# Kernel optimization log

Measured on AMD Instinct MI355X. Metric: run time of the kernel, lower is better.

The kernel has to match this reference:

```python
import jax, jax.numpy as jnp
import numpy as np

B, T, D = 64, 512, 1024   # batch, seq, input_dim
R, O = 1024, 1024          # recurrent_dim, output_dim


def setup_inputs() -> dict:
    key = jax.random.key(0)
    ks = jax.random.split(key, 8)
    s_in = 1.0 / np.sqrt(D)
    s_rec = 1.0 / np.sqrt(R)
    return {
        "x": jax.random.normal(ks[0], (B, T, D), dtype=jnp.float32),
        "Wxh": jax.random.uniform(ks[1], (R, D), jnp.float32, -s_in, s_in),
        "bh": jax.random.uniform(ks[2], (R,), jnp.float32, -s_in, s_in),
        "Whh": jax.random.uniform(ks[3], (R, R), jnp.float32, -s_rec, s_rec),
        "Wxz": jax.random.uniform(ks[4], (R, D), jnp.float32, -s_in, s_in),
        "bz": jax.random.uniform(ks[5], (R,), jnp.float32, -s_in, s_in),
        "Whz": jax.random.uniform(ks[6], (R, R), jnp.float32, -s_rec, s_rec),
        "Wy": jax.random.uniform(ks[7], (O, R), jnp.float32, -s_rec, s_rec),
        "by": jnp.zeros((O,), dtype=jnp.float32),
    }


def reference(x, Wxh, bh, Whh, Wxz, bz, Whz, Wy, by):
    # Original per-step math (note the quirk: h2z output is added to x_t
    # BEFORE x2z):
    #   z  = sigmoid(Wxz @ (x_t + Whz @ h) + bz)
    #   hb = relu(Wxh @ x_t + bh + Whh @ h)
    #   h  = z * h + (1 - z) * hb
    # Precompute all input-side GEMMs in one batched contraction (linearity);
    # fold Wxz@Whz into a single recurrent matrix.
    xh = jnp.einsum('btd,rd->btr', x, Wxh) + bh          # [B,T,R]
    xz = jnp.einsum('btd,rd->btr', x, Wxz) + bz          # [B,T,R]
    Mz = Wxz @ Whz                                        # [R,R]

    def step(h, inp):
        xh_t, xz_t = inp                                  # each [B,R]
        z = jax.nn.sigmoid(xz_t + h @ Mz.T)
        hb = jax.nn.relu(xh_t + h @ Whh.T)
        h = z * h + (1.0 - z) * hb
        return h, None

    h0 = jnp.zeros((x.shape[0], Whh.shape[0]), dtype=x.dtype)
    # scan over time: move T to leading axis
    h_final, _ = jax.lax.scan(
        step, h0, (jnp.swapaxes(xh, 0, 1), jnp.swapaxes(xz, 0, 1)))
    return h_final @ Wy.T + by                            # [B,O]
```

## Files before the change

### kernel.cpp

```cpp
#include <hip/hip_runtime.h>

#define BB 64
#define TT 512
#define DD 1024
#define RR 1024

#define SCAN_BLOCKS 32
#define HS_STRIDE 1032
#define SCAN_LDS_BYTES (64 * HS_STRIDE * 2)

typedef __bf16 bf16x8 __attribute__((ext_vector_type(8)));
typedef float f32x4 __attribute__((ext_vector_type(4)));
typedef unsigned short us4 __attribute__((ext_vector_type(4)));
typedef unsigned int u32x4 __attribute__((ext_vector_type(4)));
typedef unsigned long long u64;

__device__ inline unsigned short f2bf(float f) {
  unsigned int u = __float_as_uint(f);
  u = (u + 0x7fffu + ((u >> 16) & 1u)) >> 16;
  return (unsigned short)u;
}
__device__ inline float bf2f(unsigned short b) {
  return __uint_as_float(((unsigned int)b) << 16);
}

__device__ inline u32x4 ld16_sc(const void* p) {
  u32x4 r;
  asm volatile("global_load_dwordx4 %0, %1, off sc0 sc1"
               : "=v"(r) : "v"(p) : "memory");
  return r;
}

__global__ void k_f2b4(const float* __restrict__ in, unsigned short* __restrict__ out, int n4) {
  int i = blockIdx.x * blockDim.x + threadIdx.x;
  if (i < n4) {
    const float4 v = ((const float4*)in)[i];
    us4 o;
    o.x = f2bf(v.x); o.y = f2bf(v.y); o.z = f2bf(v.z); o.w = f2bf(v.w);
    ((us4*)out)[i] = o;
  }
}

__global__ __launch_bounds__(256) void k_transpose_bf16(
    const float* __restrict__ in, unsigned short* __restrict__ out) {
  __shared__ float tile[32][33];
  const int bx = blockIdx.x * 32, by0 = blockIdx.y * 32;
  const int tx = threadIdx.x, ty = threadIdx.y;
#pragma unroll
  for (int r = 0; r < 32; r += 8)
    tile[ty + r][tx] = in[(size_t)(by0 + ty + r) * 1024 + bx + tx];
  __syncthreads();
#pragma unroll
  for (int r = 0; r < 32; r += 8)
    out[(size_t)(bx + ty + r) * 1024 + by0 + tx] = f2bf(tile[tx][ty + r]);
}

__device__ inline void gload_lds16(const unsigned short* g, unsigned short* l) {
  __builtin_amdgcn_global_load_lds(
      (const __attribute__((address_space(1))) unsigned int*)g,
      (__attribute__((address_space(3))) unsigned int*)l, 16, 0, 0);
}

template <int EPI>
__global__ __launch_bounds__(256) void gemm_bt(
    const unsigned short* __restrict__ A,
    const unsigned short* __restrict__ Bm,
    const float* __restrict__ bias_h,
    const float* __restrict__ bias_z,
    unsigned short* __restrict__ outb, int K) {
  __shared__ __attribute__((aligned(16))) unsigned short As[128 * 32];
  __shared__ __attribute__((aligned(16))) unsigned short Bs[128 * 32];
  const int tid = threadIdx.x;
  const int m0 = blockIdx.y * 128, n0 = blockIdx.x * 128;
  const int lane = tid & 63, wid = tid >> 6;
  const int l16 = lane & 15, quad = lane >> 4;
  const int wm = (wid & 1) * 64, wn = (wid >> 1) * 64;

  f32x4 acc[4][4] = {};

  const int c0 = tid, c1 = 256 + tid;
  const int rowA0 = c0 >> 2, colA0 = (c0 & 3) << 3;
  const int rowA1 = c1 >> 2, colA1 = (c1 & 3) << 3;

  for (int kk = 0; kk < K; kk += 32) {
    __syncthreads();
    gload_lds16(A + (size_t)(m0 + rowA0) * K + kk + colA0, As + c0 * 8);
    gload_lds16(A + (size_t)(m0 + rowA1) * K + kk + colA1, As + c1 * 8);
    gload_lds16(Bm + (size_t)(n0 + rowA0) * K + kk + colA0, Bs + c0 * 8);
    gload_lds16(Bm + (size_t)(n0 + rowA1) * K + kk + colA1, Bs + c1 * 8);
    __syncthreads();
    bf16x8 af[4], bfr[4];
#pragma unroll
    for (int i = 0; i < 4; ++i) {
      af[i] = *(const bf16x8*)&As[(wm + i * 16 + l16) * 32 + quad * 8];
      bfr[i] = *(const bf16x8*)&Bs[(wn + i * 16 + l16) * 32 + quad * 8];
    }
#pragma unroll
    for (int i = 0; i < 4; ++i)
#pragma unroll
      for (int j = 0; j < 4; ++j)
        acc[i][j] = __builtin_amdgcn_mfma_f32_16x16x32_bf16(af[i], bfr[j], acc[i][j], 0, 0, 0);
  }

#pragma unroll
  for (int i = 0; i < 4; ++i) {
#pragma unroll
    for (int j = 0; j < 4; ++j) {
#pragma unroll
      for (int r = 0; r < 4; ++r) {
        const int m = m0 + wm + i * 16 + quad * 4 + r;
        const int n = n0 + wn + j * 16 + l16;
        float v = acc[i][j][r];
        if (EPI == 0) {
          v += (n < 1024) ? bias_h[n] : bias_z[n - 1024];
          const int b = m >> 9;
          const int t = m & 511;
          outb[((size_t)(t * 64 + b) << 11) + n] = f2bf(v);
        } else {
          outb[(size_t)m * 1024 + n] = f2bf(v);
        }
      }
    }
  }
}

__global__ __launch_bounds__(1024) void scan_out_k(
    const unsigned short* __restrict__ xhz,
    const unsigned short* __restrict__ Wrec,
    const unsigned short* __restrict__ Wyb,
    const float* __restrict__ by,
    unsigned short* __restrict__ hb0, unsigned short* __restrict__ hb1,
    unsigned int* __restrict__ flags,
    float* __restrict__ out) {
  extern __shared__ char smem[];
  unsigned short* hs = (unsigned short*)smem;
  float* red = (float*)smem;

  const int tid = threadIdx.x, g = blockIdx.x;
  const int lane = tid & 63, wid = tid >> 6;
  const int l16 = lane & 15, quad = lane >> 4;
  const int ks = wid >> 2, nsub = wid & 3;
  const int kw = ks * 256;
  const int i0 = g * 32;

  const int bcol = (nsub < 2) ? (i0 + nsub * 16 + l16)
                              : (1024 + i0 + (nsub - 2) * 16 + l16);
  const unsigned short* Bb = Wrec + (size_t)bcol * 1024 + kw + quad * 8;
  bf16x8 bfr[8];
#pragma unroll
  for (int s = 0; s < 8; ++s) bfr[s] = *(const bf16x8*)(Bb + s * 32);

  const int sr = tid >> 4;
  const int su = tid & 15;
  const unsigned short* gsrc_base0 = hb0 + sr * 1024 + su * 8;
  const unsigned short* gsrc_base1 = hb1 + sr * 1024 + su * 8;
  unsigned short* ldst = hs + sr * HS_STRIDE + su * 8;

  const int eb = tid >> 4, ej = (tid & 15) * 2;
  float hold0 = 0.0f, hold1 = 0.0f;

  const unsigned short* hbc = hb0;
  unsigned short* hbn = hb1;
  const unsigned short* gsrc = gsrc_base0;

  for (int tt = 0; tt < TT; ++tt) {
    u32x4 tmp[8];
#pragma unroll
    for (int c = 0; c < 8; ++c)
      tmp[c] = ld16_sc((const char*)gsrc + c * 256);
    const size_t xrow = ((size_t)(tt * 64 + eb)) << 11;
    const unsigned int xh2 = *(const unsigned int*)(xhz + xrow + i0 + ej);
    const unsigned int xz2 = *(const unsigned int*)(xhz + xrow + 1024 + i0 + ej);
    asm volatile("s_waitcnt vmcnt(0)" ::: "memory");
#pragma unroll
    for (int c = 0; c < 8; ++c)
      *(u32x4*)(ldst + c * 128) = tmp[c];
    __syncthreads();

    f32x4 acc[4] = {};
#pragma unroll
    for (int s = 0; s < 8; ++s) {
#pragma unroll
      for (int mt = 0; mt < 4; ++mt) {
        const bf16x8 afr = *(const bf16x8*)(hs + (mt * 16 + l16) * HS_STRIDE + kw + s * 32 + quad * 8);
        acc[mt] = __builtin_amdgcn_mfma_f32_16x16x32_bf16(afr, bfr[s], acc[mt], 0, 0, 0);
      }
    }
    __syncthreads();

#pragma unroll
    for (int mt = 0; mt < 4; ++mt)
#pragma unroll
      for (int r = 0; r < 4; ++r)
        red[(size_t)(ks * 64 + mt * 16 + quad * 4 + r) * 68 + nsub * 16 + l16] = acc[mt][r];
    __syncthreads();

    float ph0 = 0.f, ph1 = 0.f, pz0 = 0.f, pz1 = 0.f;
#pragma unroll
    for (int w = 0; w < 4; ++w) {
      const float* rb = red + (size_t)(w * 64 + eb) * 68;
      ph0 += rb[ej]; ph1 += rb[ej + 1];
      pz0 += rb[32 + ej]; pz1 += rb[32 + ej + 1];
    }
    {
      const float xh0 = bf2f((unsigned short)(xh2 & 0xffff));
      const float xh1 = bf2f((unsigned short)(xh2 >> 16));
      const float xz0 = bf2f((unsigned short)(xz2 & 0xffff));
      const float xz1 = bf2f((unsigned short)(xz2 >> 16));
      const float z0 = 1.0f / (1.0f + __expf(-(xz0 + pz0)));
      const float z1 = 1.0f / (1.0f + __expf(-(xz1 + pz1)));
      const float hb_0 = fmaxf(xh0 + ph0, 0.0f);
      const float hb_1 = fmaxf(xh1 + ph1, 0.0f);
      hold0 = z0 * hold0 + (1.0f - z0) * hb_0;
      hold1 = z1 * hold1 + (1.0f - z1) * hb_1;
      const unsigned int pk = (unsigned int)f2bf(hold0) | ((unsigned int)f2bf(hold1) << 16);
      __hip_atomic_store((unsigned int*)(hbn + eb * 1024 + i0 + ej), pk,
                         __ATOMIC_RELAXED, __HIP_MEMORY_SCOPE_AGENT);
    }

    __syncthreads();
    if (tid == 0)
      __hip_atomic_store(&flags[g], (unsigned int)(tt + 1),
                         __ATOMIC_RELAXED, __HIP_MEMORY_SCOPE_AGENT);
    if (tid < 64) {
      const unsigned int tgt = (unsigned int)(tt + 1);
      unsigned int v;
      do {
        v = __hip_atomic_load(&flags[tid & 31], __ATOMIC_RELAXED, __HIP_MEMORY_SCOPE_AGENT);
      } while (__any(v < tgt));
    }
    __syncthreads();

    const unsigned short* tc = hbc; hbc = hbn; hbn = (unsigned short*)tc;
    gsrc = (tt & 1) ? gsrc_base0 : gsrc_base1;
  }

  {
    u32x4 tmp[8];
#pragma unroll
    for (int c = 0; c < 8; ++c)
      tmp[c] = ld16_sc((const char*)(hbc + sr * 1024 + su * 8) + c * 256);
    asm volatile("s_waitcnt vmcnt(0)" ::: "memory");
#pragma unroll
    for (int c = 0; c < 8; ++c)
      *(u32x4*)(ldst + c * 128) = tmp[c];
  }
  __syncthreads();

  if (nsub < 2) {
    const int ocol = i0 + nsub * 16 + l16;
    const unsigned short* Byb = Wyb + (size_t)ocol * 1024 + kw + quad * 8;
    f32x4 acc[4] = {};
#pragma unroll
    for (int s = 0; s < 8; ++s) {
      const bf16x8 byf = *(const bf16x8*)(Byb + s * 32);
#pragma unroll
      for (int mt = 0; mt < 4; ++mt) {
        const bf16x8 afr = *(const bf16x8*)(hs + (mt * 16 + l16) * HS_STRIDE + kw + s * 32 + quad * 8);
        acc[mt] = __builtin_amdgcn_mfma_f32_16x16x32_bf16(afr, byf, acc[mt], 0, 0, 0);
      }
    }
    __syncthreads();
#pragma unroll
    for (int mt = 0; mt < 4; ++mt)
#pragma unroll
      for (int r = 0; r < 4; ++r)
        red[(size_t)(ks * 64 + mt * 16 + quad * 4 + r) * 68 + nsub * 16 + l16] = acc[mt][r];
  } else {
    __syncthreads();
  }
  __syncthreads();

  {
    float o0 = by[i0 + ej], o1 = by[i0 + ej + 1];
#pragma unroll
    for (int w = 0; w < 4; ++w) {
      const float* rb = red + (size_t)(w * 64 + eb) * 68;
      o0 += rb[ej]; o1 += rb[ej + 1];
    }
    float2 ov; ov.x = o0; ov.y = o1;
    *(float2*)(out + (size_t)eb * 1024 + i0 + ej) = ov;
  }
}

extern "C" void kernel_launch(void* const* d_in, const int* in_sizes, int n_in,
                              void* d_out, int out_size, void* d_ws, size_t ws_size,
                              hipStream_t stream) {
  const float* x = (const float*)d_in[0];
  const float* Wxh = (const float*)d_in[1];
  const float* bh = (const float*)d_in[2];
  const float* Whh = (const float*)d_in[3];
  const float* Wxz = (const float*)d_in[4];
  const float* bz = (const float*)d_in[5];
  const float* Whz = (const float*)d_in[6];
  const float* Wy = (const float*)d_in[7];
  const float* by = (const float*)d_in[8];
  float* out = (float*)d_out;

  char* ws = (char*)d_ws;
  size_t off = 0;
  auto alloc = [&](size_t bytes) -> void* {
    void* p = ws + off;
    off += (bytes + 255) & ~(size_t)255;
    return p;
  };
  const size_t nX = (size_t)BB * TT * DD;
  unsigned short* xb = (unsigned short*)alloc(nX * 2);
  unsigned short* Wcat = (unsigned short*)alloc((size_t)2048 * 1024 * 2);
  unsigned short* WhzT = (unsigned short*)alloc((size_t)1024 * 1024 * 2);
  unsigned short* Wrec = (unsigned short*)alloc((size_t)2048 * 1024 * 2);
  unsigned short* Wyb = (unsigned short*)alloc((size_t)1024 * 1024 * 2);
  unsigned short* xhz = (unsigned short*)alloc((size_t)TT * BB * 2048 * 2);
  unsigned short* hb0 = (unsigned short*)alloc((size_t)BB * RR * 2);
  unsigned short* hb1 = (unsigned short*)alloc((size_t)BB * RR * 2);
  unsigned int* flags = (unsigned int*)alloc(1024);

  hipMemsetAsync(hb0, 0, (size_t)BB * RR * 2, stream);
  hipMemsetAsync(flags, 0, 1024, stream);

  k_f2b4<<<dim3((unsigned)(nX / 4 / 256)), 256, 0, stream>>>(x, xb, (int)(nX / 4));
  k_f2b4<<<dim3(1024), 256, 0, stream>>>(Wxh, Wcat, 262144);
  k_f2b4<<<dim3(1024), 256, 0, stream>>>(Wxz, Wcat + 1024 * 1024, 262144);
  k_f2b4<<<dim3(1024), 256, 0, stream>>>(Whh, Wrec, 262144);
  k_f2b4<<<dim3(1024), 256, 0, stream>>>(Wy, Wyb, 262144);
  k_transpose_bf16<<<dim3(32, 32), dim3(32, 8), 0, stream>>>(Whz, WhzT);

  gemm_bt<1><<<dim3(8, 8), 256, 0, stream>>>(Wcat + 1024 * 1024, WhzT, nullptr, nullptr,
                                             Wrec + (size_t)1024 * 1024, 1024);
  gemm_bt<0><<<dim3(16, 256), 256, 0, stream>>>(xb, Wcat, bh, bz, xhz, 1024);

  hipFuncSetAttribute((const void*)scan_out_k,
                      hipFuncAttributeMaxDynamicSharedMemorySize, SCAN_LDS_BYTES);
  const unsigned short* xhz_c = xhz;
  const unsigned short* Wrec_c = Wrec;
  const unsigned short* Wyb_c = Wyb;
  const float* by_c = by;
  void* kargs[] = {(void*)&xhz_c, (void*)&Wrec_c, (void*)&Wyb_c, (void*)&by_c,
                   (void*)&hb0, (void*)&hb1, (void*)&flags, (void*)&out};
  hipLaunchCooperativeKernel((void*)scan_out_k, dim3(SCAN_BLOCKS), dim3(1024),
                             kargs, SCAN_LDS_BYTES, stream);
}
```

Baseline: 3.382 ms.

## Restructure recurrent scan: poll-before-load, direct global-to-LDS h loads, 2x2 wave tiling

Reworks the persistent scan kernel's per-step flow. The grid-wide barrier now sits at the top of each step and is split across waves, each polling only a couple of flags, instead of one wave polling all flags followed by an extra block barrier. The hidden state is loaded with global_load_lds directly into a K-major LDS layout, avoiding the register round trip and the unpadded-stride layout. Waves now compute 2x2 MFMA tiles, and only 256 threads do the gate epilogue with 16-byte stores. This cuts barrier count and latency per step, but correctness depends on the cache-bypass bits and memory ordering of the new load path. The xh extraction expression also looks odd.

```diff
diff --git a/kernel.cpp b/kernel.cpp
--- a/kernel.cpp
+++ b/kernel.cpp
@@ -6,12 +6,12 @@
 #define RR 1024
 
 #define SCAN_BLOCKS 32
-#define HS_STRIDE 1032
-#define SCAN_LDS_BYTES (64 * HS_STRIDE * 2)
+#define SCAN_LDS_BYTES 131072
 
 typedef __bf16 bf16x8 __attribute__((ext_vector_type(8)));
 typedef float f32x4 __attribute__((ext_vector_type(4)));
 typedef unsigned short us4 __attribute__((ext_vector_type(4)));
+typedef unsigned short us8 __attribute__((ext_vector_type(8)));
 typedef unsigned int u32x4 __attribute__((ext_vector_type(4)));
 typedef unsigned long long u64;
 
@@ -24,11 +24,8 @@
   return __uint_as_float(((unsigned int)b) << 16);
 }
 
-__device__ inline u32x4 ld16_sc(const void* p) {
-  u32x4 r;
-  asm volatile("global_load_dwordx4 %0, %1, off sc0 sc1"
-               : "=v"(r) : "v"(p) : "memory");
-  return r;
+__device__ inline void st16_sc(void* p, u32x4 v) {
+  asm volatile("global_store_dwordx4 %0, %1, off sc0 sc1" :: "v"(p), "v"(v) : "memory");
 }
 
 __global__ void k_f2b4(const float* __restrict__ in, unsigned short* __restrict__ out, int n4) {
@@ -59,6 +56,11 @@
   __builtin_amdgcn_global_load_lds(
       (const __attribute__((address_space(1))) unsigned int*)g,
       (__attribute__((address_space(3))) unsigned int*)l, 16, 0, 0);
+}
+__device__ inline void gload_lds16_sc(const unsigned short* g, unsigned short* l) {
+  __builtin_amdgcn_global_load_lds(
+      (const __attribute__((address_space(1))) unsigned int*)g,
+      (__attribute__((address_space(3))) unsigned int*)l, 16, 0, 17);
 }
 
 template <int EPI>
@@ -137,149 +139,166 @@
   float* red = (float*)smem;
 
   const int tid = threadIdx.x, g = blockIdx.x;
-  const int lane = tid & 63, wid = tid >> 6;
+  const int lane = tid & 63, w = tid >> 6;
   const int l16 = lane & 15, quad = lane >> 4;
-  const int ks = wid >> 2, nsub = wid & 3;
+  const int ks = w >> 2, ms = (w >> 1) & 1, ns = w & 1;
   const int kw = ks * 256;
   const int i0 = g * 32;
 
-  const int bcol = (nsub < 2) ? (i0 + nsub * 16 + l16)
-                              : (1024 + i0 + (nsub - 2) * 16 + l16);
-  const unsigned short* Bb = Wrec + (size_t)bcol * 1024 + kw + quad * 8;
-  bf16x8 bfr[8];
-#pragma unroll
-  for (int s = 0; s < 8; ++s) bfr[s] = *(const bf16x8*)(Bb + s * 32);
-
-  const int sr = tid >> 4;
-  const int su = tid & 15;
-  const unsigned short* gsrc_base0 = hb0 + sr * 1024 + su * 8;
-  const unsigned short* gsrc_base1 = hb1 + sr * 1024 + su * 8;
-  unsigned short* ldst = hs + sr * HS_STRIDE + su * 8;
-
-  const int eb = tid >> 4, ej = (tid & 15) * 2;
-  float hold0 = 0.0f, hold1 = 0.0f;
+  bf16x8 bfr[8][2];
+#pragma unroll
+  for (int nf = 0; nf < 2; ++nf) {
+    const int brow = (ns == 0) ? (i0 + nf * 16 + l16) : (1024 + i0 + nf * 16 + l16);
+    const unsigned short* Bp = Wrec + (size_t)brow * 1024 + kw + quad * 8;
+#pragma unroll
+    for (int s = 0; s < 8; ++s) bfr[s][nf] = *(const bf16x8*)(Bp + s * 32);
+  }
+
+  const int pidx = 2 * w + (lane & 1);
+  const bool polls = (lane < 2);
+
+  const int eb = tid >> 2, oc8 = (tid & 3) * 8;
+  float hold[8] = {0.f, 0.f, 0.f, 0.f, 0.f, 0.f, 0.f, 0.f};
 
   const unsigned short* hbc = hb0;
   unsigned short* hbn = hb1;
-  const unsigned short* gsrc = gsrc_base0;
 
   for (int tt = 0; tt < TT; ++tt) {
-    u32x4 tmp[8];
-#pragma unroll
-    for (int c = 0; c < 8; ++c)
-      tmp[c] = ld16_sc((const char*)gsrc + c * 256);
-    const size_t xrow = ((size_t)(tt * 64 + eb)) << 11;
-    const unsigned int xh2 = *(const unsigned int*)(xhz + xrow + i0 + ej);
-    const unsigned int xz2 = *(const unsigned int*)(xhz + xrow + 1024 + i0 + ej);
-    asm volatile("s_waitcnt vmcnt(0)" ::: "memory");
-#pragma unroll
-    for (int c = 0; c < 8; ++c)
-      *(u32x4*)(ldst + c * 128) = tmp[c];
-    __syncthreads();
-
-    f32x4 acc[4] = {};
+    {
+      const unsigned int tgt = (unsigned int)tt;
+      unsigned int v;
+      do {
+        v = polls ? __hip_atomic_load(&flags[pidx], __ATOMIC_RELAXED, __HIP_MEMORY_SCOPE_AGENT)
+                  : 0xffffffffu;
+      } while (__any(v < tgt));
+    }
+#pragma unroll
+    for (int j = 0; j < 8; ++j) {
+      const int c8 = w * 8 + j;
+      gload_lds16_sc(hbc + (size_t)lane * 1024 + c8 * 8, hs + c8 * 512);
+    }
+    u32x4 xh8 = {}, xz8 = {};
+    if (tid < 256) {
+      const size_t xrow = ((size_t)(tt * 64 + eb)) << 11;
+      xh8 = *(const u32x4*)(xhz + xrow + i0 + oc8);
+      xz8 = *(const u32x4*)(xhz + xrow + 1024 + i0 + oc8);
+    }
+    __syncthreads();
+
+    f32x4 acc[2][2] = {};
 #pragma unroll
     for (int s = 0; s < 8; ++s) {
-#pragma unroll
-      for (int mt = 0; mt < 4; ++mt) {
-        const bf16x8 afr = *(const bf16x8*)(hs + (mt * 16 + l16) * HS_STRIDE + kw + s * 32 + quad * 8);
-        acc[mt] = __builtin_amdgcn_mfma_f32_16x16x32_bf16(afr, bfr[s], acc[mt], 0, 0, 0);
-      }
-    }
-    __syncthreads();
-
-#pragma unroll
-    for (int mt = 0; mt < 4; ++mt)
-#pragma unroll
-      for (int r = 0; r < 4; ++r)
-        red[(size_t)(ks * 64 + mt * 16 + quad * 4 + r) * 68 + nsub * 16 + l16] = acc[mt][r];
-    __syncthreads();
-
-    float ph0 = 0.f, ph1 = 0.f, pz0 = 0.f, pz1 = 0.f;
-#pragma unroll
-    for (int w = 0; w < 4; ++w) {
-      const float* rb = red + (size_t)(w * 64 + eb) * 68;
-      ph0 += rb[ej]; ph1 += rb[ej + 1];
-      pz0 += rb[32 + ej]; pz1 += rb[32 + ej + 1];
-    }
-    {
-      const float xh0 = bf2f((unsigned short)(xh2 & 0xffff));
-      const float xh1 = bf2f((unsigned short)(xh2 >> 16));
-      const float xz0 = bf2f((unsigned short)(xz2 & 0xffff));
-      const float xz1 = bf2f((unsigned short)(xz2 >> 16));
-      const float z0 = 1.0f / (1.0f + __expf(-(xz0 + pz0)));
-      const float z1 = 1.0f / (1.0f + __expf(-(xz1 + pz1)));
-      const float hb_0 = fmaxf(xh0 + ph0, 0.0f);
-      const float hb_1 = fmaxf(xh1 + ph1, 0.0f);
-      hold0 = z0 * hold0 + (1.0f - z0) * hb_0;
-      hold1 = z1 * hold1 + (1.0f - z1) * hb_1;
-      const unsigned int pk = (unsigned int)f2bf(hold0) | ((unsigned int)f2bf(hold1) << 16);
-      __hip_atomic_store((unsigned int*)(hbn + eb * 1024 + i0 + ej), pk,
-                         __ATOMIC_RELAXED, __HIP_MEMORY_SCOPE_AGENT);
-    }
-
+      const int c8 = ks * 32 + s * 4 + quad;
+#pragma unroll
+      for (int mt = 0; mt < 2; ++mt) {
+        const int row = ms * 32 + mt * 16 + l16;
+        const bf16x8 afr = *(const bf16x8*)(hs + c8 * 512 + row * 8);
+        acc[mt][0] = __builtin_amdgcn_mfma_f32_16x16x32_bf16(afr, bfr[s][0], acc[mt][0], 0, 0, 0);
+        acc[mt][1] = __builtin_amdgcn_mfma_f32_16x16x32_bf16(afr, bfr[s][1], acc[mt][1], 0, 0, 0);
+      }
+    }
+    __syncthreads();
+
+#pragma unroll
+    for (int mt = 0; mt < 2; ++mt)
+#pragma unroll
+      for (int nf = 0; nf < 2; ++nf)
+#pragma unroll
+        for (int r = 0; r < 4; ++r)
+          red[(size_t)(ks * 64 + ms * 32 + mt * 16 + quad * 4 + r) * 68 +
+              ns * 32 + nf * 16 + l16] = acc[mt][nf][r];
+    __syncthreads();
+
+    if (tid < 256) {
+      float ph[8] = {}, pz[8] = {};
+#pragma unroll
+      for (int k = 0; k < 4; ++k) {
+        const float* rb = red + (size_t)(k * 64 + eb) * 68;
+        const float4 a0 = *(const float4*)(rb + oc8);
+        const float4 a1 = *(const float4*)(rb + oc8 + 4);
+        const float4 c0 = *(const float4*)(rb + 32 + oc8);
+        const float4 c1 = *(const float4*)(rb + 32 + oc8 + 4);
+        ph[0] += a0.x; ph[1] += a0.y; ph[2] += a0.z; ph[3] += a0.w;
+        ph[4] += a1.x; ph[5] += a1.y; ph[6] += a1.z; ph[7] += a1.w;
+        pz[0] += c0.x; pz[1] += c0.y; pz[2] += c0.z; pz[3] += c0.w;
+        pz[4] += c1.x; pz[5] += c1.y; pz[6] += c1.z; pz[7] += c1.w;
+      }
+      unsigned short hb16[8];
+#pragma unroll
+      for (int j = 0; j < 8; ++j) {
+        const float xh = bf2f((unsigned short)((j < 4 ? xh8[j] : 0), ((const unsigned short*)&xh8)[j]));
+        const float xz = bf2f(((const unsigned short*)&xz8)[j]);
+        const float z = 1.0f / (1.0f + __expf(-(xz + pz[j])));
+        const float hbv = fmaxf(xh + ph[j], 0.0f);
+        hold[j] = z * hold[j] + (1.0f - z) * hbv;
+        hb16[j] = f2bf(hold[j]);
+      }
+      u32x4 pk;
+#pragma unroll
+      for (int j = 0; j < 4; ++j)
+        pk[j] = (unsigned int)hb16[2 * j] | ((unsigned int)hb16[2 * j + 1] << 16);
+      st16_sc(hbn + (size_t)eb * 1024 + i0 + oc8, pk);
+    }
     __syncthreads();
     if (tid == 0)
       __hip_atomic_store(&flags[g], (unsigned int)(tt + 1),
                          __ATOMIC_RELAXED, __HIP_MEMORY_SCOPE_AGENT);
-    if (tid < 64) {
-      const unsigned int tgt = (unsigned int)(tt + 1);
-      unsigned int v;
-      do {
-        v = __hip_atomic_load(&flags[tid & 31], __ATOMIC_RELAXED, __HIP_MEMORY_SCOPE_AGENT);
-      } while (__any(v < tgt));
-    }
-    __syncthreads();
 
     const unsigned short* tc = hbc; hbc = hbn; hbn = (unsigned short*)tc;
-    gsrc = (tt & 1) ? gsrc_base0 : gsrc_base1;
   }
 
   {
-    u32x4 tmp[8];
-#pragma unroll
-    for (int c = 0; c < 8; ++c)
-      tmp[c] = ld16_sc((const char*)(hbc + sr * 1024 + su * 8) + c * 256);
-    asm volatile("s_waitcnt vmcnt(0)" ::: "memory");
-#pragma unroll
-    for (int c = 0; c < 8; ++c)
-      *(u32x4*)(ldst + c * 128) = tmp[c];
+    const unsigned int tgt = (unsigned int)TT;
+    unsigned int v;
+    do {
+      v = polls ? __hip_atomic_load(&flags[pidx], __ATOMIC_RELAXED, __HIP_MEMORY_SCOPE_AGENT)
+                : 0xffffffffu;
+    } while (__any(v < tgt));
+  }
+#pragma unroll
+  for (int j = 0; j < 8; ++j) {
+    const int c8 = w * 8 + j;
+    gload_lds16_sc(hbc + (size_t)lane * 1024 + c8 * 8, hs + c8 * 512);
   }
   __syncthreads();
 
-  if (nsub < 2) {
-    const int ocol = i0 + nsub * 16 + l16;
-    const unsigned short* Byb = Wyb + (size_t)ocol * 1024 + kw + quad * 8;
-    f32x4 acc[4] = {};
+  {
+    const int ocol = i0 + ns * 16 + l16;
+    const unsigned short* Byp = Wyb + (size_t)ocol * 1024 + kw + quad * 8;
+    bf16x8 bfr2[8];
+#pragma unroll
+    for (int s = 0; s < 8; ++s) bfr2[s] = *(const bf16x8*)(Byp + s * 32);
+    f32x4 acc2[2] = {};
 #pragma unroll
     for (int s = 0; s < 8; ++s) {
-      const bf16x8 byf = *(const bf16x8*)(Byb + s * 32);
-#pragma unroll
-      for (int mt = 0; mt < 4; ++mt) {
-        const bf16x8 afr = *(const bf16x8*)(hs + (mt * 16 + l16) * HS_STRIDE + kw + s * 32 + quad * 8);
-        acc[mt] = __builtin_amdgcn_mfma_f32_16x16x32_bf16(afr, byf, acc[mt], 0, 0, 0);
-      }
-    }
-    __syncthreads();
-#pragma unroll
-    for (int mt = 0; mt < 4; ++mt)
+      const int c8 = ks * 32 + s * 4 + quad;
+#pragma unroll
+      for (int mt = 0; mt < 2; ++mt) {
+        const int row = ms * 32 + mt * 16 + l16;
+        const bf16x8 afr = *(const bf16x8*)(hs + c8 * 512 + row * 8);
+        acc2[mt] = __builtin_amdgcn_mfma_f32_16x16x32_bf16(afr, bfr2[s], acc2[mt], 0, 0, 0);
+      }
+    }
+    __syncthreads();
+    float* red2 = (float*)smem;
+#pragma unroll
+    for (int mt = 0; mt < 2; ++mt)
 #pragma unroll
       for (int r = 0; r < 4; ++r)
-        red[(size_t)(ks * 64 + mt * 16 + quad * 4 + r) * 68 + nsub * 16 + l16] = acc[mt][r];
-  } else {
-    __syncthreads();
+        red2[(size_t)(ks * 64 + ms * 32 + mt * 16 + quad * 4 + r) * 36 + ns * 16 + l16] = acc2[mt][r];
   }
   __syncthreads();
-
   {
-    float o0 = by[i0 + ej], o1 = by[i0 + ej + 1];
-#pragma unroll
-    for (int w = 0; w < 4; ++w) {
-      const float* rb = red + (size_t)(w * 64 + eb) * 68;
-      o0 += rb[ej]; o1 += rb[ej + 1];
+    float* red2 = (float*)smem;
+    const int b = tid >> 4, oc2 = (tid & 15) * 2;
+    float o0 = by[i0 + oc2], o1 = by[i0 + oc2 + 1];
+#pragma unroll
+    for (int k = 0; k < 4; ++k) {
+      const float* rb = red2 + (size_t)(k * 64 + b) * 36;
+      o0 += rb[oc2]; o1 += rb[oc2 + 1];
     }
     float2 ov; ov.x = o0; ov.y = o1;
-    *(float2*)(out + (size_t)eb * 1024 + i0 + ej) = ov;
+    *(float2*)(out + (size_t)b * 1024 + i0 + oc2) = ov;
   }
 }
 
```

Result: slower. 5.596 ms (+65.5%).
